# Performance work log

Hardware: AMD Instinct MI355X
Metric: run time of the kernel (lower is better)

Reference implementation:

```python
import jax, jax.numpy as jnp
import numpy as np

E = 1024
H = 16
D = E // H
B = 4
T = 2048


def setup_inputs() -> dict:
    key = jax.random.key(0)
    ks = jax.random.split(key, 12)
    s = 0.02
    inp = {
        "query": jax.random.normal(ks[0], (B, T, E), jnp.float32),
        "key_in": jax.random.normal(ks[1], (B, T, E), jnp.float32),
        "value": jax.random.normal(ks[2], (B, T, E), jnp.float32),
        "mask": jnp.tril(jnp.ones((T, T), jnp.int32))[None, None, :, :],
        "Wq": jax.random.normal(ks[3], (E, E), jnp.float32) * s,
        "bq": jnp.zeros((E,), jnp.float32),
        "Wk": jax.random.normal(ks[4], (E, E), jnp.float32) * s,
        "bk": jnp.zeros((E,), jnp.float32),
        "Wv": jax.random.normal(ks[5], (E, E), jnp.float32) * s,
        "bv": jnp.zeros((E,), jnp.float32),
        "Wo": jax.random.normal(ks[6], (E, E), jnp.float32) * s,
        "bo": jnp.zeros((E,), jnp.float32),
    }
    return inp


def _shape(x):
    # [B, T, E] -> [B, H, T, D]
    return x.reshape(B, -1, H, D).transpose(0, 2, 1, 3)


def reference(query, key_in, value, mask, Wq, bq, Wk, bk, Wv, bv, Wo, bo):
    q = _shape(query @ Wq.T + bq)
    k = _shape(key_in @ Wk.T + bk)
    v = _shape(value @ Wv.T + bv)
    scale = 1.0 / jnp.sqrt(jnp.float32(D))
    # [B, H, Tq, Tk]
    scores = jnp.einsum("bhqd,bhkd->bhqk", q, k) * scale
    scores = jnp.where(mask == 0, jnp.float32(-jnp.inf), scores)
    attn = jax.nn.softmax(scores, axis=-1)
    out = jnp.einsum("bhqk,bhkd->bhqd", attn, v)
    out = out.transpose(0, 2, 1, 3).reshape(B, T, E)
    return out @ Wo.T + bo
```

## Files before the change

### kernel.cpp

```cpp
#include <hip/hip_runtime.h>
#include <hip/hip_bf16.h>
#include <cstdint>

#define BB 4
#define TT 2048
#define EE 1024
#define HH 16
#define DD 64
#define BH (BB*HH)
#define MM (BB*TT)
#define KK 1024
#define KSTR 72
#define VSTR 136
#define LOG2E 1.44269504088896340736f

typedef __attribute__((ext_vector_type(8))) short short8;
typedef __attribute__((ext_vector_type(4))) short short4_;
typedef __attribute__((ext_vector_type(4))) float float4_;
typedef __attribute__((ext_vector_type(4))) ushort ushort4_;

__device__ __forceinline__ void gl_lds16(const void* g, void* l) {
    __builtin_amdgcn_global_load_lds(
        (const __attribute__((address_space(1))) void*)g,
        (__attribute__((address_space(3))) void*)l, 16, 0, 0);
}

__device__ __forceinline__ ushort f2bf(float v) {
    __hip_bfloat16 h = __float2bfloat16(v);
    return *(ushort*)&h;
}

__global__ __launch_bounds__(256) void cvt_kernel(
    const float* __restrict__ s0, ushort* __restrict__ d0, int n0,
    const float* __restrict__ s1, ushort* __restrict__ d1, int n1,
    const float* __restrict__ s2, ushort* __restrict__ d2, int n2,
    const float* __restrict__ s3, ushort* __restrict__ d3, int n3)
{
    const float* s; ushort* d; int n;
    switch (blockIdx.y) {
        case 0: s = s0; d = d0; n = n0; break;
        case 1: s = s1; d = d1; n = n1; break;
        case 2: s = s2; d = d2; n = n2; break;
        default: s = s3; d = d3; n = n3; break;
    }
    int i = (blockIdx.x * 256 + threadIdx.x) * 4;
    if (i >= n) return;
    float4_ v = *(const float4_*)&s[i];
    ushort4_ o;
#pragma unroll
    for (int j = 0; j < 4; j++) o[j] = f2bf(v[j]);
    *(ushort4_*)&d[i] = o;
}

template<int MODE>
__global__ __launch_bounds__(256, 3) void gemm_nt(
    const ushort* __restrict__ A, const ushort* __restrict__ W,
    const float* __restrict__ bias, void* __restrict__ Cout, float scale)
{
    __shared__ __align__(16) ushort As[128*32];
    __shared__ __align__(16) ushort Bs[128*32];

    const int tid  = threadIdx.x;
    const int wave = tid >> 6;
    const int lane = tid & 63;
    const int l15  = lane & 15;
    const int quad = lane >> 4;
    const int wm   = wave & 1;
    const int wn   = wave >> 1;

    const long rowBase = (long)blockIdx.y * 128;
    const long colBase = (long)blockIdx.x * 128;

    float4_ acc[4][4];
#pragma unroll
    for (int i = 0; i < 4; i++)
#pragma unroll
        for (int j = 0; j < 4; j++) acc[i][j] = float4_{0.f, 0.f, 0.f, 0.f};

    for (int k0 = 0; k0 < KK; k0 += 32) {
        __syncthreads();
#pragma unroll
        for (int it = 0; it < 2; it++) {
            int idx = it * 256 + tid;
            int r   = idx >> 2;
            int c8  = (idx & 3) * 8;
            gl_lds16(A + (rowBase + r) * KK + k0 + c8, &As[idx * 8]);
            gl_lds16(W + (colBase + r) * KK + k0 + c8, &Bs[idx * 8]);
        }
        __syncthreads();

        short8 af[4], bf[4];
#pragma unroll
        for (int mt = 0; mt < 4; mt++)
            af[mt] = *(const short8*)&As[(wm*64 + mt*16 + l15) * 32 + quad*8];
#pragma unroll
        for (int nt = 0; nt < 4; nt++)
            bf[nt] = *(const short8*)&Bs[(wn*64 + nt*16 + l15) * 32 + quad*8];
#pragma unroll
        for (int mt = 0; mt < 4; mt++)
#pragma unroll
            for (int nt = 0; nt < 4; nt++)
                acc[mt][nt] = __builtin_amdgcn_mfma_f32_16x16x32_bf16(
                    af[mt], bf[nt], acc[mt][nt], 0, 0, 0);
    }

#pragma unroll
    for (int nt = 0; nt < 4; nt++) {
        const long col = colBase + wn*64 + nt*16 + l15;
        const float bv = bias[col];
#pragma unroll
        for (int mt = 0; mt < 4; mt++) {
            const long row0 = rowBase + wm*64 + mt*16 + quad*4;
            if (MODE == 2) {
                const long h = col >> 6, d = col & (DD - 1);
                const long b = row0 >> 11, t0 = row0 & (TT - 1);
                ushort4_ pk;
#pragma unroll
                for (int i = 0; i < 4; i++) pk[i] = f2bf((acc[mt][nt][i] + bv) * scale);
                *(ushort4_*)((ushort*)Cout + ((b*HH + h)*DD + d)*TT + t0) = pk;
            } else {
#pragma unroll
                for (int i = 0; i < 4; i++) {
                    const long row = row0 + i;
                    const float v = (acc[mt][nt][i] + bv) * scale;
                    if (MODE == 0) {
                        ((float*)Cout)[row * EE + col] = v;
                    } else {
                        const long b = row >> 11, t = row & (TT - 1);
                        const long h = col >> 6,  d = col & (DD - 1);
                        ((ushort*)Cout)[(((b*HH + h) * TT) + t) * DD + d] = f2bf(v);
                    }
                }
            }
        }
    }
}

__global__ __launch_bounds__(512, 4) void flash_kernel(
    const ushort* __restrict__ Qh, const ushort* __restrict__ Kh,
    const ushort* __restrict__ Vt, ushort* __restrict__ AO)
{
    __shared__ __align__(16) ushort Ks[128*KSTR];
    __shared__ __align__(16) ushort Vs[64*VSTR];

    const int qt  = (TT/128 - 1) - blockIdx.x;
    const int bh  = blockIdx.y;
    const int tid = threadIdx.x;
    const int wave = tid >> 6, lane = tid & 63;
    const int l15 = lane & 15, quad = lane >> 4;

    const ushort* Qb = Qh + (long)bh * TT * DD;
    const ushort* Kb = Kh + (long)bh * TT * DD;
    const ushort* Vb = Vt + (long)bh * DD * TT;

    const int qrow = qt*128 + wave*16 + l15;
    short8 aq0 = *(const short8*)&Qb[(long)qrow * DD + quad*8];
    short8 aq1 = *(const short8*)&Qb[(long)qrow * DD + 32 + quad*8];

    float4_ o[4];
#pragma unroll
    for (int nt = 0; nt < 4; nt++) o[nt] = float4_{0.f, 0.f, 0.f, 0.f};
    float m_run = -INFINITY, l_run = 0.0f;

    const int nkt = qt + 1;

    short8 kreg[2], vreg[2];
#pragma unroll
    for (int it = 0; it < 2; it++) {
        int c = it * 512 + tid;
        int kk = c >> 3, ks = c & 7;
        kreg[it] = *(const short8*)&Kb[(long)kk * DD + ks*8];
        int dd = c >> 4, vs = c & 15;
        vreg[it] = *(const short8*)&Vb[(long)dd * TT + vs*8];
    }

    for (int kt = 0; kt < nkt; kt++) {
        __syncthreads();
#pragma unroll
        for (int it = 0; it < 2; it++) {
            int c = it * 512 + tid;
            int kk = c >> 3, ks = c & 7;
            *(short8*)&Ks[kk*KSTR + ks*8] = kreg[it];
            int dd = c >> 4, vs = c & 15;
            *(short8*)&Vs[dd*VSTR + vs*8] = vreg[it];
        }
        __syncthreads();

        if (kt + 1 < nkt) {
            const long koff = (long)(kt+1) * 128;
#pragma unroll
            for (int it = 0; it < 2; it++) {
                int c = it * 512 + tid;
                int kk = c >> 3, ks = c & 7;
                kreg[it] = *(const short8*)&Kb[(koff + kk) * DD + ks*8];
                int dd = c >> 4, vs = c & 15;
                vreg[it] = *(const short8*)&Vb[(long)dd * TT + koff + vs*8];
            }
        }

        float4_ s[8];
        __builtin_amdgcn_s_setprio(1);
#pragma unroll
        for (int nt = 0; nt < 8; nt++) {
            short8 bk0 = *(const short8*)&Ks[(nt*16 + l15) * KSTR + quad*8];
            short8 bk1 = *(const short8*)&Ks[(nt*16 + l15) * KSTR + 32 + quad*8];
            float4_ acc = float4_{0.f, 0.f, 0.f, 0.f};
            acc = __builtin_amdgcn_mfma_f32_16x16x32_bf16(bk0, aq0, acc, 0,0,0);
            acc = __builtin_amdgcn_mfma_f32_16x16x32_bf16(bk1, aq1, acc, 0,0,0);
            s[nt] = acc;
        }
        __builtin_amdgcn_s_setprio(0);

        if (kt == nkt - 1) {
#pragma unroll
            for (int nt = 0; nt < 8; nt++) {
#pragma unroll
                for (int i = 0; i < 4; i++) {
                    const int key = kt*128 + nt*16 + quad*4 + i;
                    if (key > qrow) s[nt][i] = -INFINITY;
                }
            }
        }

        float t8[8];
#pragma unroll
        for (int nt = 0; nt < 8; nt++)
            t8[nt] = fmaxf(fmaxf(s[nt][0], s[nt][1]), fmaxf(s[nt][2], s[nt][3]));
        float pm = fmaxf(fmaxf(fmaxf(t8[0], t8[1]), fmaxf(t8[2], t8[3])),
                         fmaxf(fmaxf(t8[4], t8[5]), fmaxf(t8[6], t8[7])));
        pm = fmaxf(pm, __shfl_xor(pm, 16));
        pm = fmaxf(pm, __shfl_xor(pm, 32));

        if (!__all(pm <= m_run + 8.0f)) {
            const float mnew = fmaxf(m_run, pm);
            const float alpha = exp2f(m_run - mnew);
            m_run = mnew;
            l_run *= alpha;
#pragma unroll
            for (int nt = 0; nt < 4; nt++)
#pragma unroll
                for (int i = 0; i < 4; i++) o[nt][i] *= alpha;
        }

        float rs0 = 0.f, rs1 = 0.f, rs2 = 0.f, rs3 = 0.f;
        short8 pb[4];
#pragma unroll
        for (int c = 0; c < 4; c++) {
#pragma unroll
            for (int half = 0; half < 2; half++) {
                const int nt = 2*c + half;
                const float p0 = exp2f(s[nt][0] - m_run);
                const float p1 = exp2f(s[nt][1] - m_run);
                const float p2 = exp2f(s[nt][2] - m_run);
                const float p3 = exp2f(s[nt][3] - m_run);
                rs0 += p0; rs1 += p1; rs2 += p2; rs3 += p3;
                pb[c][half*4 + 0] = (short)f2bf(p0);
                pb[c][half*4 + 1] = (short)f2bf(p1);
                pb[c][half*4 + 2] = (short)f2bf(p2);
                pb[c][half*4 + 3] = (short)f2bf(p3);
            }
        }
        float rs = (rs0 + rs1) + (rs2 + rs3);
        rs += __shfl_xor(rs, 16);
        rs += __shfl_xor(rs, 32);
        l_run += rs;

        __builtin_amdgcn_s_setprio(1);
#pragma unroll
        for (int c = 0; c < 4; c++) {
            const short8 bp = pb[c];
#pragma unroll
            for (int nt = 0; nt < 4; nt++) {
                const ushort* vrow = &Vs[(nt*16 + l15) * VSTR];
                short4_ lo = *(const short4_*)&vrow[(2*c    )*16 + quad*4];
                short4_ hi = *(const short4_*)&vrow[(2*c + 1)*16 + quad*4];
                short8 av;
                av[0]=lo[0]; av[1]=lo[1]; av[2]=lo[2]; av[3]=lo[3];
                av[4]=hi[0]; av[5]=hi[1]; av[6]=hi[2]; av[7]=hi[3];
                o[nt] = __builtin_amdgcn_mfma_f32_16x16x32_bf16(av, bp, o[nt], 0,0,0);
            }
        }
        __builtin_amdgcn_s_setprio(0);
    }

    const int h = bh & (HH - 1);
    const int b = bh >> 4;
    const float inv = 1.0f / l_run;
    const long rowOff = ((long)(b*TT + qrow)) * EE + h*64;
#pragma unroll
    for (int nt = 0; nt < 4; nt++) {
        ushort4_ pk;
#pragma unroll
        for (int i = 0; i < 4; i++) pk[i] = f2bf(o[nt][i] * inv);
        *(ushort4_*)&AO[rowOff + nt*16 + quad*4] = pk;
    }
}

extern "C" void kernel_launch(void* const* d_in, const int* in_sizes, int n_in,
                              void* d_out, int out_size, void* d_ws, size_t ws_size,
                              hipStream_t stream)
{
    const float* query  = (const float*)d_in[0];
    const float* key_in = (const float*)d_in[1];
    const float* value  = (const float*)d_in[2];
    const float* Wq = (const float*)d_in[4];
    const float* bq = (const float*)d_in[5];
    const float* Wk = (const float*)d_in[6];
    const float* bk = (const float*)d_in[7];
    const float* Wv = (const float*)d_in[8];
    const float* bv = (const float*)d_in[9];
    const float* Wo = (const float*)d_in[10];
    const float* bo = (const float*)d_in[11];

    ushort* ws = (ushort*)d_ws;
    const size_t NIN = (size_t)MM * KK;
    const size_t NW  = (size_t)EE * KK;
    ushort* X0  = ws;
    ushort* Wqc = ws + NIN;
    ushort* Wkc = Wqc + NW;
    ushort* Wvc = Wkc + NW;
    ushort* Woc = Wvc + NW;
    ushort* Qh  = Woc + NW;
    ushort* Kh  = Qh + NIN;
    ushort* Vth = Kh + NIN;
    ushort* AO  = X0;

    dim3 gemm_grid(EE/128, MM/128);
    const dim3 cvtW_grid(NW/1024, 4), cvtI_grid(NIN/1024, 1);

    cvt_kernel<<<cvtW_grid, 256, 0, stream>>>(Wq, Wqc, (int)NW, Wk, Wkc, (int)NW,
                                              Wv, Wvc, (int)NW, Wo, Woc, (int)NW);
    cvt_kernel<<<cvtI_grid, 256, 0, stream>>>(query, X0, (int)NIN, nullptr, nullptr, 0,
                                              nullptr, nullptr, 0, nullptr, nullptr, 0);
    gemm_nt<1><<<gemm_grid, 256, 0, stream>>>(X0, Wqc, bq, Qh, 0.125f * LOG2E);
    cvt_kernel<<<cvtI_grid, 256, 0, stream>>>(key_in, X0, (int)NIN, nullptr, nullptr, 0,
                                              nullptr, nullptr, 0, nullptr, nullptr, 0);
    gemm_nt<1><<<gemm_grid, 256, 0, stream>>>(X0, Wkc, bk, Kh, 1.0f);
    cvt_kernel<<<cvtI_grid, 256, 0, stream>>>(value, X0, (int)NIN, nullptr, nullptr, 0,
                                              nullptr, nullptr, 0, nullptr, nullptr, 0);
    gemm_nt<2><<<gemm_grid, 256, 0, stream>>>(X0, Wvc, bv, Vth, 1.0f);

    flash_kernel<<<dim3(TT/128, BH), 512, 0, stream>>>(Qh, Kh, Vth, AO);
    gemm_nt<0><<<gemm_grid, 256, 0, stream>>>(AO, Woc, bo, d_out, 1.0f);
}
```

Before: 421.3 us.

## Fuse fp32-to-bf16 input conversion into projection GEMM loads with register prefetch

Removes the three standalone conversion kernels for query/key/value by having the projection GEMMs read fp32 activations directly and convert to bf16 in registers. It replaces the async global-to-LDS loads with register-staged loads that prefetch the next K tile while MFMAs run on the current one. This avoids writing and re-reading a bf16 copy of each input and saves three launches. In exchange, each GEMM tile now reads twice the bytes for A and redoes the conversion for every column block. It also uses more registers, which may hurt occupancy.

```diff
diff --git a/kernel.cpp b/kernel.cpp
--- a/kernel.cpp
+++ b/kernel.cpp
@@ -18,12 +18,6 @@
 typedef __attribute__((ext_vector_type(4))) short short4_;
 typedef __attribute__((ext_vector_type(4))) float float4_;
 typedef __attribute__((ext_vector_type(4))) ushort ushort4_;
-
-__device__ __forceinline__ void gl_lds16(const void* g, void* l) {
-    __builtin_amdgcn_global_load_lds(
-        (const __attribute__((address_space(1))) void*)g,
-        (__attribute__((address_space(3))) void*)l, 16, 0, 0);
-}
 
 __device__ __forceinline__ ushort f2bf(float v) {
     __hip_bfloat16 h = __float2bfloat16(v);
@@ -52,9 +46,9 @@
     *(ushort4_*)&d[i] = o;
 }
 
-template<int MODE>
+template<int MODE, bool AF32>
 __global__ __launch_bounds__(256, 3) void gemm_nt(
-    const ushort* __restrict__ A, const ushort* __restrict__ W,
+    const void* __restrict__ Ain, const ushort* __restrict__ W,
     const float* __restrict__ bias, void* __restrict__ Cout, float scale)
 {
     __shared__ __align__(16) ushort As[128*32];
@@ -71,6 +65,33 @@
     const long rowBase = (long)blockIdx.y * 128;
     const long colBase = (long)blockIdx.x * 128;
 
+    int sr[2], sc[2];
+#pragma unroll
+    for (int it = 0; it < 2; it++) {
+        int idx = it * 256 + tid;
+        sr[it] = idx >> 2;
+        sc[it] = (idx & 3) * 8;
+    }
+
+    short8 pa[2], pw[2];
+
+#pragma unroll
+    for (int it = 0; it < 2; it++) {
+        if (AF32) {
+            const float* Arow = (const float*)Ain + (rowBase + sr[it]) * KK + sc[it];
+            float4_ f0 = *(const float4_*)&Arow[0];
+            float4_ f1 = *(const float4_*)&Arow[4];
+#pragma unroll
+            for (int j = 0; j < 4; j++) {
+                pa[it][j]     = (short)f2bf(f0[j]);
+                pa[it][j + 4] = (short)f2bf(f1[j]);
+            }
+        } else {
+            pa[it] = *(const short8*)((const ushort*)Ain + (rowBase + sr[it]) * KK + sc[it]);
+        }
+        pw[it] = *(const short8*)&W[(colBase + sr[it]) * KK + sc[it]];
+    }
+
     float4_ acc[4][4];
 #pragma unroll
     for (int i = 0; i < 4; i++)
@@ -82,12 +103,30 @@
 #pragma unroll
         for (int it = 0; it < 2; it++) {
             int idx = it * 256 + tid;
-            int r   = idx >> 2;
-            int c8  = (idx & 3) * 8;
-            gl_lds16(A + (rowBase + r) * KK + k0 + c8, &As[idx * 8]);
-            gl_lds16(W + (colBase + r) * KK + k0 + c8, &Bs[idx * 8]);
+            *(short8*)&As[idx * 8] = pa[it];
+            *(short8*)&Bs[idx * 8] = pw[it];
         }
         __syncthreads();
+
+        if (k0 + 32 < KK) {
+            const int kn = k0 + 32;
+#pragma unroll
+            for (int it = 0; it < 2; it++) {
+                if (AF32) {
+                    const float* Arow = (const float*)Ain + (rowBase + sr[it]) * KK + kn + sc[it];
+                    float4_ f0 = *(const float4_*)&Arow[0];
+                    float4_ f1 = *(const float4_*)&Arow[4];
+#pragma unroll
+                    for (int j = 0; j < 4; j++) {
+                        pa[it][j]     = (short)f2bf(f0[j]);
+                        pa[it][j + 4] = (short)f2bf(f1[j]);
+                    }
+                } else {
+                    pa[it] = *(const short8*)((const ushort*)Ain + (rowBase + sr[it]) * KK + kn + sc[it]);
+                }
+                pw[it] = *(const short8*)&W[(colBase + sr[it]) * KK + kn + sc[it]];
+            }
+        }
 
         short8 af[4], bf[4];
 #pragma unroll
@@ -315,31 +354,25 @@
     ushort* ws = (ushort*)d_ws;
     const size_t NIN = (size_t)MM * KK;
     const size_t NW  = (size_t)EE * KK;
-    ushort* X0  = ws;
-    ushort* Wqc = ws + NIN;
+    ushort* Wqc = ws;
     ushort* Wkc = Wqc + NW;
     ushort* Wvc = Wkc + NW;
     ushort* Woc = Wvc + NW;
     ushort* Qh  = Woc + NW;
     ushort* Kh  = Qh + NIN;
     ushort* Vth = Kh + NIN;
-    ushort* AO  = X0;
+    ushort* AO  = Vth + NIN;
 
     dim3 gemm_grid(EE/128, MM/128);
-    const dim3 cvtW_grid(NW/1024, 4), cvtI_grid(NIN/1024, 1);
+    const dim3 cvtW_grid(NW/1024, 4);
 
     cvt_kernel<<<cvtW_grid, 256, 0, stream>>>(Wq, Wqc, (int)NW, Wk, Wkc, (int)NW,
                                               Wv, Wvc, (int)NW, Wo, Woc, (int)NW);
-    cvt_kernel<<<cvtI_grid, 256, 0, stream>>>(query, X0, (int)NIN, nullptr, nullptr, 0,
-                                              nullptr, nullptr, 0, nullptr, nullptr, 0);
-    gemm_nt<1><<<gemm_grid, 256, 0, stream>>>(X0, Wqc, bq, Qh, 0.125f * LOG2E);
-    cvt_kernel<<<cvtI_grid, 256, 0, stream>>>(key_in, X0, (int)NIN, nullptr, nullptr, 0,
-                                              nullptr, nullptr, 0, nullptr, nullptr, 0);
-    gemm_nt<1><<<gemm_grid, 256, 0, stream>>>(X0, Wkc, bk, Kh, 1.0f);
-    cvt_kernel<<<cvtI_grid, 256, 0, stream>>>(value, X0, (int)NIN, nullptr, nullptr, 0,
-                                              nullptr, nullptr, 0, nullptr, nullptr, 0);
-    gemm_nt<2><<<gemm_grid, 256, 0, stream>>>(X0, Wvc, bv, Vth, 1.0f);
+    gemm_nt<1, true><<<gemm_grid, 256, 0, stream>>>(query,  Wqc, bq, Qh,  0.125f * LOG2E);
+    gemm_nt<1, true><<<gemm_grid, 256, 0, stream>>>(key_in, Wkc, bk, Kh,  1.0f);
+    gemm_nt<2, true><<<gemm_grid, 256, 0, stream>>>(value,  Wvc, bv, Vth, 1.0f);
 
     flash_kernel<<<dim3(TT/128, BH), 512, 0, stream>>>(Qh, Kh, Vth, AO);
-    gemm_nt<0><<<gemm_grid, 256, 0, stream>>>(AO, Woc, bo, d_out, 1.0f);
-}
+
+    gemm_nt<0, false><<<gemm_grid, 256, 0, stream>>>(AO, Woc, bo, d_out, 1.0f);
+}
```

Result: slower. 438.5 us (+4.1%).
